# Performance work log

Hardware: AMD Instinct MI355X
Metric: run time of the kernel (lower is better)

Reference implementation:

```python
import jax, jax.numpy as jnp
import numpy as np

N = 30000
DEG = 16
E_RAND = N * DEG
E = E_RAND + N  # with self loops appended
T = 2
F_IN, H1, OUT = 128, 128, 64
NBSZ = 15
AGG = 0.8
NEG_SLOPE = 0.2


def setup_inputs() -> dict:
    key = jax.random.key(0)
    ks = jax.random.split(key, 10)
    x_all = jax.random.normal(ks[0], (T, N, F_IN), dtype=jnp.float32)
    # edges per snapshot: random edges + self loops (mirrors remove_self_loops + add_self_loops)
    loops = jnp.arange(N, dtype=jnp.int32)
    eis = []
    for t in range(T):
        src = jax.random.randint(jax.random.fold_in(ks[1], t), (E_RAND,), 0, N, dtype=jnp.int32)
        dst = jax.random.randint(jax.random.fold_in(ks[2], t), (E_RAND,), 0, N, dtype=jnp.int32)
        eis.append(jnp.stack([jnp.concatenate([src, loops]), jnp.concatenate([dst, loops])]))
    edge_index_all = jnp.stack(eis)  # [T, 2, E]
    def glorot(k, shape):
        fan = shape[0] + shape[-1]
        s = jnp.sqrt(6.0 / fan)
        return jax.random.uniform(k, shape, jnp.float32, -s, s)
    W1 = glorot(ks[3], (F_IN, 2 * H1))
    att1 = glorot(ks[4], (1, 1, 4 * H1))   # [1, heads=1, 2*out_neurons]
    b1 = jnp.zeros((2 * H1,), jnp.float32)
    W2 = glorot(ks[5], (H1, 2 * OUT))
    att2 = glorot(ks[6], (1, 1, 4 * OUT))
    b2 = jnp.zeros((2 * OUT,), jnp.float32)
    return {"x_all": x_all, "edge_index_all": edge_index_all,
            "W1": W1, "att1": att1, "b1": b1, "W2": W2, "att2": att2, "b2": b2}


def _conv(x, edge_index, W, att, b, C):
    """One DGIBConv (heads=1, Bernoulli distribution, diag reparam, eval mode).
    Returns (node_out [N,C], ixz scalar, structure_kl scalar)."""
    h = x @ W                                    # [N, 2C]
    src, dst = edge_index[0], edge_index[1]
    x_j = h[src]                                 # [E, 2C] per-edge gather (source)
    x_i = h[dst]                                 # [E, 2C] target
    a = att[0, 0]                                # [4C]
    logits = jnp.sum(x_i * a[:2 * C], -1) + jnp.sum(x_j * a[2 * C:], -1)  # [E]
    logits = jax.nn.leaky_relu(logits, NEG_SLOPE)
    # Bernoulli branch: softmax of ones over segments == 1/deg(dst)
    deg = jax.ops.segment_sum(jnp.ones_like(logits), dst, num_segments=N)  # [N]
    norm = 1.0 / deg[dst]
    p = jnp.clip(jax.nn.sigmoid(logits), 0.01, 0.99)  # posterior Bernoulli probs
    alpha = p * norm
    aggr = jax.ops.segment_sum(x_j * alpha[:, None], dst, num_segments=N) + b  # [N, 2C]
    # diag reparam: mean || std-logit split; Gaussian prior N(0, I)
    mu = aggr[:, :C]
    std = jax.nn.softplus(aggr[:, C:]) + 1e-10
    kl = -jnp.log(std) + 0.5 * (std * std + mu * mu) - 0.5  # KL(N(mu,std)||N(0,1)) per dim
    ixz = jnp.mean(jnp.sum(kl, -1))
    # structure KL: Bernoulli(p) || Bernoulli(logits = 1/nbsz)
    q = jax.nn.sigmoid(jnp.float32(1.0 / NBSZ))
    skl = jnp.mean(p * jnp.log(p / q) + (1.0 - p) * jnp.log((1.0 - p) / (1.0 - q)))
    return mu, ixz, skl


def _layer(x_list, edge_index_all, W, att, b, C):
    """Temporal DGIBConv.forward: per-snapshot conv + weighted temporal fusion."""
    outs, ixzs, skls = [], [], []
    for t in range(T):
        out, ixz, skl = _conv(x_list[t], edge_index_all[t], W, att, b, C)
        if t > 0:
            w = jax.nn.sigmoid(jnp.arange(t, dtype=jnp.float32))[:, None, None]  # [t,1,1]
            prev = jnp.stack(outs[:t])                                           # [t,N,C]
            out = jnp.sum(w * prev, 0) / t * AGG + out * (1.0 - AGG)
        outs.append(out)
        ixzs.append(ixz)
        skls.append(skl)
    return outs, jnp.mean(jnp.stack(ixzs)), jnp.mean(jnp.stack(skls))


def reference(x_all, edge_index_all, W1, att1, b1, W2, att2, b2):
    xs = [x_all[t] for t in range(T)]
    h1, ixz1, skl1 = _layer(xs, edge_index_all, W1, att1, b1, H1)
    h1 = [jax.nn.relu(h) for h in h1]  # with_relu=True, eval -> dropout is identity
    h2, ixz2, skl2 = _layer(h1, edge_index_all, W2, att2, b2, OUT)
    out = jnp.stack(h2)                # [T, N, OUT]
    ixz_mean = (ixz1 + ixz2) / 2.0
    skl_mean = (skl1 + skl2) / 2.0
    return out, ixz_mean, skl_mean
```

## Files before the change

### kernel.cpp

```cpp
#include <hip/hip_runtime.h>
#include <hip/hip_bf16.h>

#define N_NODES 30000
#define N_EDGES 510000
#define K_DIM   128
#define ABLK    7500
#define EBLK    997

typedef short bf16x8 __attribute__((ext_vector_type(8)));
typedef float f32x4  __attribute__((ext_vector_type(4)));
typedef float f32x2  __attribute__((ext_vector_type(2)));
typedef unsigned int u32x2 __attribute__((ext_vector_type(2)));

__device__ __forceinline__ unsigned short f2bf(float f) {
  __hip_bfloat16 h = __float2bfloat16(f);
  return *(unsigned short*)&h;
}

__global__ void transpose_w_kernel(const float* __restrict__ W1, unsigned short* __restrict__ Wt1,
                                   const float* __restrict__ W2, unsigned short* __restrict__ Wt2) {
  int i = blockIdx.x * blockDim.x + threadIdx.x;
  if (i < 128 * 256) {
    int k = i >> 8, m = i & 255;
    Wt1[m * 128 + k] = f2bf(W1[i]);
  } else if (i < 128 * 256 + 128 * 128) {
    int j = i - 128 * 256;
    int k = j >> 7, m = j & 127;
    Wt2[m * 128 + k] = f2bf(W2[j]);
  }
}

__global__ void deg_kernel(const int* __restrict__ ei, int* __restrict__ deg0,
                           int* __restrict__ deg1, int e) {
  int i = blockIdx.x * blockDim.x + threadIdx.x;
  if (i < 2 * e) {
    int t = i >= e ? 1 : 0;
    int j = i - t * e;
    int d = ei[(size_t)t * 2 * e + e + j];
    atomicAdd(&(t ? deg1 : deg0)[d], 1);
  }
}

__global__ __launch_bounds__(1024) void scan_kernel(const int* __restrict__ deg0, int* __restrict__ off0,
                                                    int* __restrict__ cur0, float* __restrict__ rn0,
                                                    const int* __restrict__ deg1, int* __restrict__ off1,
                                                    int* __restrict__ cur1, float* __restrict__ rn1,
                                                    int n) {
  const int* deg = blockIdx.x ? deg1 : deg0;
  int* off = blockIdx.x ? off1 : off0;
  int* cur = blockIdx.x ? cur1 : cur0;
  float* rn = blockIdx.x ? rn1 : rn0;
  const int CHUNK = 30;
  __shared__ int wsum[16];
  int tid = threadIdx.x;
  int base = tid * CHUNK;
  int sum = 0;
  for (int i = 0; i < CHUNK; i++)
    if (base + i < n) sum += deg[base + i];
  int lane = tid & 63, wid = tid >> 6;
  int incl = sum;
#pragma unroll
  for (int o = 1; o < 64; o <<= 1) {
    int v = __shfl_up(incl, o);
    if (lane >= o) incl += v;
  }
  if (lane == 63) wsum[wid] = incl;
  __syncthreads();
  if (tid == 0) {
    int run = 0;
    for (int w = 0; w < 16; w++) { int v = wsum[w]; wsum[w] = run; run += v; }
  }
  __syncthreads();
  int run = incl - sum + wsum[wid];
  for (int i = 0; i < CHUNK; i++) {
    if (base + i < n) {
      int dg = deg[base + i];
      off[base + i] = run;
      cur[base + i] = run;
      rn[base + i] = 1.0f / (float)dg;
      run += dg;
    }
  }
}

__global__ void scatter_kernel(const int* __restrict__ ei,
                               int* __restrict__ cur0, int* __restrict__ cur1,
                               unsigned int* __restrict__ csr0, unsigned int* __restrict__ csr1, int e) {
  int i = blockIdx.x * blockDim.x + threadIdx.x;
  if (i < 2 * e) {
    int t = i >= e ? 1 : 0;
    int j = i - t * e;
    int s = ei[(size_t)t * 2 * e + j];
    int d = ei[(size_t)t * 2 * e + e + j];
    int* cur = t ? cur1 : cur0;
    unsigned int* csr = t ? csr1 : csr0;
    int p = atomicAdd(&cur[d], 1);
    csr[p] = (unsigned int)s | ((unsigned int)d << 16);
  }
}

template<int M, bool F32IN>
__global__ __launch_bounds__(256) void gemm_kernel(const void* __restrict__ X0v,
                                                   const void* __restrict__ X1v,
                                                   const short* __restrict__ Wt,
                                                   unsigned char* __restrict__ H0,
                                                   unsigned char* __restrict__ H1,
                                                   const float* __restrict__ att,
                                                   float* __restrict__ si0, float* __restrict__ si1,
                                                   float* __restrict__ sj0, float* __restrict__ sj1,
                                                   int nrows) {
  int t = blockIdx.y;
  const void* Xv = t ? X1v : X0v;
  unsigned char* Hf8 = t ? H1 : H0;
  float* s_i = t ? si1 : si0;
  float* s_j = t ? sj1 : sj0;

  int wave = blockIdx.x * 4 + (threadIdx.x >> 6);
  int lane = threadIdx.x & 63;
  if (wave * 16 >= nrows) return;
  int m16 = lane & 15, quad = lane >> 4;

  bf16x8 a[4];
  size_t arow = (size_t)(wave * 16 + m16) * K_DIM + quad * 8;
  if constexpr (F32IN) {
    const float* X = (const float*)Xv;
#pragma unroll
    for (int kc = 0; kc < 4; kc++) {
      f32x4 lo = *(const f32x4*)(X + arow + kc * 32);
      f32x4 hi = *(const f32x4*)(X + arow + kc * 32 + 4);
#pragma unroll
      for (int j = 0; j < 4; j++) {
        ((unsigned short*)&a[kc])[j]     = f2bf(lo[j]);
        ((unsigned short*)&a[kc])[4 + j] = f2bf(hi[j]);
      }
    }
  } else {
    const short* X = (const short*)Xv;
#pragma unroll
    for (int kc = 0; kc < 4; kc++) a[kc] = *(const bf16x8*)(X + arow + kc * 32);
  }

  float sip[4] = {0.f, 0.f, 0.f, 0.f}, sjp[4] = {0.f, 0.f, 0.f, 0.f};
#pragma unroll
  for (int nt = 0; nt < M / 16; nt++) {
    f32x4 acc = {0.f, 0.f, 0.f, 0.f};
    size_t brow = (size_t)(nt * 16 + m16) * K_DIM + quad * 8;
#pragma unroll
    for (int kc = 0; kc < 4; kc++) {
      bf16x8 b = *(const bf16x8*)(Wt + brow + kc * 32);
      acc = __builtin_amdgcn_mfma_f32_16x16x32_bf16(a[kc], b, acc, 0, 0, 0);
    }
    int col = nt * 16 + m16;
    float aA = att[col], aB = att[M + col];
#pragma unroll
    for (int r = 0; r < 4; r++) {
      int row = wave * 16 + quad * 4 + r;
      int pk = __builtin_amdgcn_cvt_pk_fp8_f32(acc[r], acc[r], 0, false);
      Hf8[(size_t)row * M + col] = (unsigned char)pk;
      sip[r] += acc[r] * aA;
      sjp[r] += acc[r] * aB;
    }
  }
#pragma unroll
  for (int o = 1; o < 16; o <<= 1) {
#pragma unroll
    for (int r = 0; r < 4; r++) {
      sip[r] += __shfl_xor(sip[r], o);
      sjp[r] += __shfl_xor(sjp[r], o);
    }
  }
  if (m16 == 0) {
#pragma unroll
    for (int r = 0; r < 4; r++) {
      int row = wave * 16 + quad * 4 + r;
      s_i[row] = sip[r];
      s_j[row] = sjp[r];
    }
  }
}

__global__ __launch_bounds__(256) void edge_kernel(const unsigned int* __restrict__ csr_0,
                                                   const unsigned int* __restrict__ csr_1,
                                                   const float* __restrict__ rn0, const float* __restrict__ rn1,
                                                   const float* __restrict__ si0, const float* __restrict__ si1,
                                                   const float* __restrict__ sj0, const float* __restrict__ sj1,
                                                   u32x2* __restrict__ iw0, u32x2* __restrict__ iw1,
                                                   float* __restrict__ epart,
                                                   int e) {
  int t = blockIdx.y;
  const unsigned int* csr = t ? csr_1 : csr_0;
  const float* rn = t ? rn1 : rn0;
  const float* s_i = t ? si1 : si0;
  const float* s_j = t ? sj1 : sj0;
  u32x2* iw = t ? iw1 : iw0;

  const float q   = 1.0f / (1.0f + __expf(-(1.0f / 15.0f)));
  const float lq  = __logf(q);
  const float l1q = __logf(1.0f - q);

  __shared__ float red[4];
  float skl = 0.f;
  int p0 = (blockIdx.x * 256 + threadIdx.x) * 2;
#pragma unroll
  for (int u = 0; u < 2; u++) {
    int p = p0 + u;
    if (p < e) {
      unsigned int sd = csr[p];
      int s = (int)(sd & 0xffffu);
      int dd = (int)(sd >> 16);
      float lg = s_i[dd] + s_j[s];
      lg = lg > 0.f ? lg : 0.2f * lg;
      float pv = 1.0f / (1.0f + __expf(-lg));
      pv = fminf(fmaxf(pv, 0.01f), 0.99f);
      skl += pv * (__logf(pv) - lq) + (1.0f - pv) * (__logf(1.0f - pv) - l1q);
      float w = pv * rn[dd];
      u32x2 o;
      o[0] = (unsigned int)s;
      o[1] = __float_as_uint(w);
      iw[p] = o;
    }
  }
  int lane = threadIdx.x & 63, wid = threadIdx.x >> 6;
#pragma unroll
  for (int o = 32; o > 0; o >>= 1) skl += __shfl_xor(skl, o);
  if (lane == 0) red[wid] = skl;
  __syncthreads();
  if (threadIdx.x == 0) epart[t * EBLK + blockIdx.x] = red[0] + red[1] + red[2] + red[3];
}

template<int M>
__global__ __launch_bounds__(256, 6) void aggr_kernel(const unsigned char* __restrict__ H0,
                                                   const unsigned char* __restrict__ H1,
                                                   const u32x2* __restrict__ iw0, const u32x2* __restrict__ iw1,
                                                   const int* __restrict__ off0, const int* __restrict__ off1,
                                                   const int* __restrict__ deg0, const int* __restrict__ deg1,
                                                   const float* __restrict__ bias,
                                                   float* __restrict__ mu0, float* __restrict__ mu1,
                                                   float* __restrict__ apart,
                                                   int n) {
  constexpr int C = M / 2;
  constexpr int LPR = M / 8;
  constexpr int L2LPR = (M == 256) ? 5 : 4;
  constexpr int EPL = 64 / LPR;
  constexpr int NL = 8;
  constexpr int U = NL * EPL;

  int t = blockIdx.y;
  const unsigned char* Hf8 = t ? H1 : H0;
  const u32x2* iw = t ? iw1 : iw0;
  const int* off = t ? off1 : off0;
  const int* deg = t ? deg1 : deg0;
  float* mu = t ? mu1 : mu0;

  __shared__ float red_i[4];
  int wid = threadIdx.x >> 6, lane = threadIdx.x & 63;
  int wave = blockIdx.x * 4 + wid;
  float ixz = 0.f;

  if (wave < n) {
    int d     = __builtin_amdgcn_readfirstlane(deg[wave]);
    int start = __builtin_amdgcn_readfirstlane(off[wave]);
    const u32x2* iwp = iw + start;
    int sub = lane & (LPR - 1);
    int g   = lane >> L2LPR;
    int c0  = sub * 8;
    const unsigned char* hbase = Hf8 + c0;

    f32x2 acc[4];
#pragma unroll
    for (int k = 0; k < 4; k++) acc[k] = {0.f, 0.f};

    for (int e0 = 0; e0 < d; e0 += U) {
      u32x2 iwl[NL];
#pragma unroll
      for (int l = 0; l < NL; l++) {
        int e = e0 + l * EPL + g;
        iwl[l] = iwp[e < d ? e : d - 1];
      }
      u32x2 hv[NL];
#pragma unroll
      for (int l = 0; l < NL; l++)
        hv[l] = *(const u32x2*)(hbase + (size_t)iwl[l][0] * M);
#pragma unroll
      for (int l = 0; l < NL; l++) {
        int e = e0 + l * EPL + g;
        float wf = (e < d) ? __uint_as_float(iwl[l][1]) : 0.f;
        f32x2 wv = {wf, wf};
        f32x2 d0 = __builtin_amdgcn_cvt_pk_f32_fp8((int)hv[l][0], false);
        f32x2 d1 = __builtin_amdgcn_cvt_pk_f32_fp8((int)hv[l][0], true);
        f32x2 d2 = __builtin_amdgcn_cvt_pk_f32_fp8((int)hv[l][1], false);
        f32x2 d3 = __builtin_amdgcn_cvt_pk_f32_fp8((int)hv[l][1], true);
        acc[0] = d0 * wv + acc[0];
        acc[1] = d1 * wv + acc[1];
        acc[2] = d2 * wv + acc[2];
        acc[3] = d3 * wv + acc[3];
      }
    }

#pragma unroll
    for (int o = LPR; o < 64; o <<= 1) {
#pragma unroll
      for (int j = 0; j < 4; j++) {
        acc[j][0] += __shfl_xor(acc[j][0], o);
        acc[j][1] += __shfl_xor(acc[j][1], o);
      }
    }

    if (lane < LPR) {
      if (c0 < C) {
        f32x4 mv[2];
#pragma unroll
        for (int j = 0; j < 4; j++) {
          float a0 = acc[j][0] + bias[c0 + 2 * j];
          float a1 = acc[j][1] + bias[c0 + 2 * j + 1];
          ixz += 0.5f * (a0 * a0 + a1 * a1) - 1.0f;
          mv[j >> 1][(j & 1) * 2]     = a0;
          mv[j >> 1][(j & 1) * 2 + 1] = a1;
        }
        *(f32x4*)(mu + (size_t)wave * C + c0)     = mv[0];
        *(f32x4*)(mu + (size_t)wave * C + c0 + 4) = mv[1];
      } else {
#pragma unroll
        for (int j = 0; j < 4; j++) {
#pragma unroll
          for (int h = 0; h < 2; h++) {
            float a = acc[j][h] + bias[c0 + 2 * j + h];
            float sp = (a > 20.f) ? a : log1pf(__expf(a));
            sp += 1e-10f;
            ixz += -__logf(sp) + 0.5f * sp * sp;
          }
        }
      }
    }
  }
#pragma unroll
  for (int o = 32; o > 0; o >>= 1) ixz += __shfl_xor(ixz, o);
  if (lane == 0) red_i[wid] = ixz;
  __syncthreads();
  if (threadIdx.x == 0)
    apart[t * ABLK + blockIdx.x] = red_i[0] + red_i[1] + red_i[2] + red_i[3];
}

__global__ void fuse1_kernel(const float* __restrict__ mu0, const float* __restrict__ mu1,
                             __hip_bfloat16* __restrict__ x0, __hip_bfloat16* __restrict__ x1, int n) {
  int i = blockIdx.x * blockDim.x + threadIdx.x;
  if (i < n) {
    float m0 = mu0[i], m1 = mu1[i];
    x0[i] = __float2bfloat16(fmaxf(m0, 0.f));
    x1[i] = __float2bfloat16(fmaxf(0.4f * m0 + 0.2f * m1, 0.f));
  }
}

__global__ void fuse2_kernel(const float* __restrict__ mu0, const float* __restrict__ mu1,
                             float* __restrict__ out, int n) {
  int i = blockIdx.x * blockDim.x + threadIdx.x;
  if (i < n) {
    float m0 = mu0[i], m1 = mu1[i];
    out[i] = m0;
    out[n + i] = 0.4f * m0 + 0.2f * m1;
  }
}

__global__ __launch_bounds__(1024) void reduce_kernel(const float* __restrict__ a1,
                                                      const float* __restrict__ a2,
                                                      const float* __restrict__ e1,
                                                      const float* __restrict__ e2,
                                                      float* __restrict__ out2) {
  __shared__ float ri[16], rs[16];
  float ixz = 0.f, skl = 0.f;
  for (int i = threadIdx.x; i < 2 * ABLK; i += 1024) ixz += a1[i] + a2[i];
  for (int i = threadIdx.x; i < 2 * EBLK; i += 1024) skl += e1[i] + e2[i];
  int lane = threadIdx.x & 63, wid = threadIdx.x >> 6;
#pragma unroll
  for (int o = 32; o > 0; o >>= 1) {
    ixz += __shfl_xor(ixz, o);
    skl += __shfl_xor(skl, o);
  }
  if (lane == 0) { ri[wid] = ixz; rs[wid] = skl; }
  __syncthreads();
  if (threadIdx.x == 0) {
    float si = 0.f, ss = 0.f;
    for (int w = 0; w < 16; w++) { si += ri[w]; ss += rs[w]; }
    out2[0] = si / (4.0f * (float)N_NODES);
    out2[1] = ss / (4.0f * (float)N_EDGES);
  }
}

extern "C" void kernel_launch(void* const* d_in, const int* in_sizes, int n_in,
                              void* d_out, int out_size, void* d_ws, size_t ws_size,
                              hipStream_t stream) {
  const float* x_all = (const float*)d_in[0];
  const int* ei      = (const int*)d_in[1];
  const float* W1    = (const float*)d_in[2];
  const float* att1  = (const float*)d_in[3];
  const float* b1    = (const float*)d_in[4];
  const float* W2    = (const float*)d_in[5];
  const float* att2  = (const float*)d_in[6];
  const float* b2    = (const float*)d_in[7];
  float* out         = (float*)d_out;

  char* ws = (char*)d_ws;
  size_t off = 0;
  auto alloc = [&](size_t bytes) {
    char* p = ws + off;
    off = (off + bytes + 255) & ~(size_t)255;
    return p;
  };
  unsigned short* wt1  = (unsigned short*)alloc(256 * 128 * sizeof(short));
  unsigned short* wt2  = (unsigned short*)alloc(128 * 128 * sizeof(short));
  unsigned char* hf8_0 = (unsigned char*)alloc((size_t)N_NODES * 256);
  unsigned char* hf8_1 = (unsigned char*)alloc((size_t)N_NODES * 256);
  float* si0   = (float*)alloc(N_NODES * sizeof(float));
  float* si1   = (float*)alloc(N_NODES * sizeof(float));
  float* sj0   = (float*)alloc(N_NODES * sizeof(float));
  float* sj1   = (float*)alloc(N_NODES * sizeof(float));
  float* mu1_0 = (float*)alloc((size_t)N_NODES * 128 * sizeof(float));
  float* mu1_1 = (float*)alloc((size_t)N_NODES * 128 * sizeof(float));
  char* x2region = alloc((size_t)N_NODES * 256 * sizeof(short));
  __hip_bfloat16* x2_0 = (__hip_bfloat16*)x2region;
  __hip_bfloat16* x2_1 = x2_0 + (size_t)N_NODES * 128;
  u32x2* iwp[2] = {(u32x2*)x2region, (u32x2*)x2region + N_EDGES};
  float* mu2_0 = mu1_0;
  float* mu2_1 = mu1_0 + (size_t)N_NODES * 64;
  int* degp[2]  = {(int*)alloc(N_NODES * 4), (int*)alloc(N_NODES * 4)};
  int* offp[2]  = {(int*)alloc(N_NODES * 4), (int*)alloc(N_NODES * 4)};
  int* curp[2]  = {(int*)alloc(N_NODES * 4), (int*)alloc(N_NODES * 4)};
  float* rnp[2] = {(float*)alloc(N_NODES * 4), (float*)alloc(N_NODES * 4)};
  unsigned int* csrp[2] = {(unsigned int*)alloc((size_t)N_EDGES * 4),
                           (unsigned int*)alloc((size_t)N_EDGES * 4)};
  float* apart1 = (float*)alloc(2 * ABLK * sizeof(float));
  float* apart2 = (float*)alloc(2 * ABLK * sizeof(float));
  float* epart1 = (float*)alloc(2 * EBLK * sizeof(float));
  float* epart2 = (float*)alloc(2 * EBLK * sizeof(float));

  hipMemsetAsync(degp[0], 0, N_NODES * 4, stream);
  hipMemsetAsync(degp[1], 0, N_NODES * 4, stream);

  transpose_w_kernel<<<192, 256, 0, stream>>>(W1, wt1, W2, wt2);

  deg_kernel<<<(2 * N_EDGES + 255) / 256, 256, 0, stream>>>(ei, degp[0], degp[1], N_EDGES);
  scan_kernel<<<2, 1024, 0, stream>>>(degp[0], offp[0], curp[0], rnp[0],
                                      degp[1], offp[1], curp[1], rnp[1], N_NODES);
  scatter_kernel<<<(2 * N_EDGES + 255) / 256, 256, 0, stream>>>(ei, curp[0], curp[1],
                                                                csrp[0], csrp[1], N_EDGES);

  dim3 ggrid(469, 2), egrid(EBLK, 2), agrid(ABLK, 2);

  const float* x0 = x_all;
  const float* x1 = x_all + (size_t)N_NODES * K_DIM;
  gemm_kernel<256, true><<<ggrid, 256, 0, stream>>>(x0, x1, (const short*)wt1, hf8_0, hf8_1,
                                                    att1, si0, si1, sj0, sj1, N_NODES);
  edge_kernel<<<egrid, 256, 0, stream>>>(csrp[0], csrp[1], rnp[0], rnp[1],
                                         si0, si1, sj0, sj1, iwp[0], iwp[1], epart1, N_EDGES);
  aggr_kernel<256><<<agrid, 256, 0, stream>>>(hf8_0, hf8_1, iwp[0], iwp[1], offp[0], offp[1],
                                              degp[0], degp[1], b1, mu1_0, mu1_1, apart1, N_NODES);
  fuse1_kernel<<<(N_NODES * 128 + 255) / 256, 256, 0, stream>>>(mu1_0, mu1_1, x2_0, x2_1, N_NODES * 128);

  gemm_kernel<128, false><<<ggrid, 256, 0, stream>>>(x2_0, x2_1, (const short*)wt2, hf8_0, hf8_1,
                                                     att2, si0, si1, sj0, sj1, N_NODES);
  edge_kernel<<<egrid, 256, 0, stream>>>(csrp[0], csrp[1], rnp[0], rnp[1],
                                         si0, si1, sj0, sj1, iwp[0], iwp[1], epart2, N_EDGES);
  aggr_kernel<128><<<agrid, 256, 0, stream>>>(hf8_0, hf8_1, iwp[0], iwp[1], offp[0], offp[1],
                                              degp[0], degp[1], b2, mu2_0, mu2_1, apart2, N_NODES);
  fuse2_kernel<<<(N_NODES * 64 + 255) / 256, 256, 0, stream>>>(mu2_0, mu2_1, out, N_NODES * 64);
  reduce_kernel<<<1, 1024, 0, stream>>>(apart1, apart2, epart1, epart2, out + (size_t)2 * N_NODES * 64);
}
```

Before: 607.6 us.

## Replace pull-based CSR gather aggregation with source-sorted push scatter using bf16 atomics

New measurement: 1.501 ms. +147.0%, slower.

```diff
diff --git a/kernel.cpp b/kernel.cpp
--- a/kernel.cpp
+++ b/kernel.cpp
@@ -1,20 +1,43 @@
 #include <hip/hip_runtime.h>
 #include <hip/hip_bf16.h>
+
+#ifndef __has_builtin
+#define __has_builtin(x) 0
+#endif
 
 #define N_NODES 30000
 #define N_EDGES 510000
 #define K_DIM   128
 #define ABLK    7500
 #define EBLK    997
+#define FB1     15000
+#define FB2     7500
 
 typedef short bf16x8 __attribute__((ext_vector_type(8)));
 typedef float f32x4  __attribute__((ext_vector_type(4)));
 typedef float f32x2  __attribute__((ext_vector_type(2)));
 typedef unsigned int u32x2 __attribute__((ext_vector_type(2)));
+typedef short s16x2 __attribute__((ext_vector_type(2)));
 
 __device__ __forceinline__ unsigned short f2bf(float f) {
   __hip_bfloat16 h = __float2bfloat16(f);
   return *(unsigned short*)&h;
+}
+__device__ __forceinline__ float bf2f(unsigned short u) {
+  __hip_bfloat16 h = *(__hip_bfloat16*)&u;
+  return __bfloat162float(h);
+}
+
+__device__ __forceinline__ void atom_pk_bf16(unsigned int* addr, float lo, float hi) {
+  __hip_bfloat162 b2(__float2bfloat16(lo), __float2bfloat16(hi));
+#if __has_builtin(__builtin_amdgcn_global_atomic_fadd_v2bf16)
+  union { __hip_bfloat162 b; s16x2 v; } u;
+  u.b = b2;
+  __builtin_amdgcn_global_atomic_fadd_v2bf16(
+      (__attribute__((address_space(1))) s16x2*)addr, u.v);
+#else
+  unsafeAtomicAdd((__hip_bfloat162*)addr, b2);
+#endif
 }
 
 __global__ void transpose_w_kernel(const float* __restrict__ W1, unsigned short* __restrict__ Wt1,
@@ -30,25 +53,29 @@
   }
 }
 
-__global__ void deg_kernel(const int* __restrict__ ei, int* __restrict__ deg0,
-                           int* __restrict__ deg1, int e) {
+__global__ void deg_kernel(const int* __restrict__ ei,
+                           int* __restrict__ deg0, int* __restrict__ deg1,
+                           int* __restrict__ degS0, int* __restrict__ degS1, int e) {
   int i = blockIdx.x * blockDim.x + threadIdx.x;
   if (i < 2 * e) {
     int t = i >= e ? 1 : 0;
     int j = i - t * e;
+    int s = ei[(size_t)t * 2 * e + j];
     int d = ei[(size_t)t * 2 * e + e + j];
     atomicAdd(&(t ? deg1 : deg0)[d], 1);
-  }
-}
-
-__global__ __launch_bounds__(1024) void scan_kernel(const int* __restrict__ deg0, int* __restrict__ off0,
-                                                    int* __restrict__ cur0, float* __restrict__ rn0,
-                                                    const int* __restrict__ deg1, int* __restrict__ off1,
-                                                    int* __restrict__ cur1, float* __restrict__ rn1,
+    atomicAdd(&(t ? degS1 : degS0)[s], 1);
+  }
+}
+
+__global__ __launch_bounds__(1024) void scan_kernel(const int* __restrict__ degS0, int* __restrict__ offS0, int* __restrict__ curS0,
+                                                    const int* __restrict__ degS1, int* __restrict__ offS1, int* __restrict__ curS1,
+                                                    const int* __restrict__ deg0, float* __restrict__ rn0,
+                                                    const int* __restrict__ deg1, float* __restrict__ rn1,
                                                     int n) {
+  const int* degS = blockIdx.x ? degS1 : degS0;
+  int* off = blockIdx.x ? offS1 : offS0;
+  int* cur = blockIdx.x ? curS1 : curS0;
   const int* deg = blockIdx.x ? deg1 : deg0;
-  int* off = blockIdx.x ? off1 : off0;
-  int* cur = blockIdx.x ? cur1 : cur0;
   float* rn = blockIdx.x ? rn1 : rn0;
   const int CHUNK = 30;
   __shared__ int wsum[16];
@@ -56,7 +83,7 @@
   int base = tid * CHUNK;
   int sum = 0;
   for (int i = 0; i < CHUNK; i++)
-    if (base + i < n) sum += deg[base + i];
+    if (base + i < n) sum += degS[base + i];
   int lane = tid & 63, wid = tid >> 6;
   int incl = sum;
 #pragma unroll
@@ -74,27 +101,27 @@
   int run = incl - sum + wsum[wid];
   for (int i = 0; i < CHUNK; i++) {
     if (base + i < n) {
-      int dg = deg[base + i];
+      int dg = degS[base + i];
       off[base + i] = run;
       cur[base + i] = run;
-      rn[base + i] = 1.0f / (float)dg;
+      rn[base + i] = 1.0f / (float)deg[base + i];
       run += dg;
     }
   }
 }
 
 __global__ void scatter_kernel(const int* __restrict__ ei,
-                               int* __restrict__ cur0, int* __restrict__ cur1,
-                               unsigned int* __restrict__ csr0, unsigned int* __restrict__ csr1, int e) {
+                               int* __restrict__ curS0, int* __restrict__ curS1,
+                               unsigned int* __restrict__ csrS0, unsigned int* __restrict__ csrS1, int e) {
   int i = blockIdx.x * blockDim.x + threadIdx.x;
   if (i < 2 * e) {
     int t = i >= e ? 1 : 0;
     int j = i - t * e;
     int s = ei[(size_t)t * 2 * e + j];
     int d = ei[(size_t)t * 2 * e + e + j];
-    int* cur = t ? cur1 : cur0;
-    unsigned int* csr = t ? csr1 : csr0;
-    int p = atomicAdd(&cur[d], 1);
+    int* cur = t ? curS1 : curS0;
+    unsigned int* csr = t ? csrS1 : csrS0;
+    int p = atomicAdd(&cur[s], 1);
     csr[p] = (unsigned int)s | ((unsigned int)d << 16);
   }
 }
@@ -215,7 +242,7 @@
       skl += pv * (__logf(pv) - lq) + (1.0f - pv) * (__logf(1.0f - pv) - l1q);
       float w = pv * rn[dd];
       u32x2 o;
-      o[0] = (unsigned int)s;
+      o[0] = (unsigned int)dd;
       o[1] = __float_as_uint(w);
       iw[p] = o;
     }
@@ -229,136 +256,112 @@
 }
 
 template<int M>
-__global__ __launch_bounds__(256, 6) void aggr_kernel(const unsigned char* __restrict__ H0,
+__global__ __launch_bounds__(256) void scat_kernel(const unsigned char* __restrict__ H0,
                                                    const unsigned char* __restrict__ H1,
                                                    const u32x2* __restrict__ iw0, const u32x2* __restrict__ iw1,
-                                                   const int* __restrict__ off0, const int* __restrict__ off1,
-                                                   const int* __restrict__ deg0, const int* __restrict__ deg1,
-                                                   const float* __restrict__ bias,
-                                                   float* __restrict__ mu0, float* __restrict__ mu1,
-                                                   float* __restrict__ apart,
+                                                   const int* __restrict__ offS0, const int* __restrict__ offS1,
+                                                   const int* __restrict__ degS0, const int* __restrict__ degS1,
+                                                   unsigned short* __restrict__ A0, unsigned short* __restrict__ A1v,
                                                    int n) {
-  constexpr int C = M / 2;
-  constexpr int LPR = M / 8;
-  constexpr int L2LPR = (M == 256) ? 5 : 4;
-  constexpr int EPL = 64 / LPR;
-  constexpr int NL = 8;
-  constexpr int U = NL * EPL;
-
   int t = blockIdx.y;
   const unsigned char* Hf8 = t ? H1 : H0;
   const u32x2* iw = t ? iw1 : iw0;
-  const int* off = t ? off1 : off0;
-  const int* deg = t ? deg1 : deg0;
-  float* mu = t ? mu1 : mu0;
-
-  __shared__ float red_i[4];
+  const int* offS = t ? offS1 : offS0;
+  const int* degS = t ? degS1 : degS0;
+  unsigned int* A = (unsigned int*)(t ? A1v : A0);
+
   int wid = threadIdx.x >> 6, lane = threadIdx.x & 63;
-  int wave = blockIdx.x * 4 + wid;
-  float ixz = 0.f;
-
-  if (wave < n) {
-    int d     = __builtin_amdgcn_readfirstlane(deg[wave]);
-    int start = __builtin_amdgcn_readfirstlane(off[wave]);
-    const u32x2* iwp = iw + start;
-    int sub = lane & (LPR - 1);
-    int g   = lane >> L2LPR;
-    int c0  = sub * 8;
-    const unsigned char* hbase = Hf8 + c0;
-
-    f32x2 acc[4];
-#pragma unroll
-    for (int k = 0; k < 4; k++) acc[k] = {0.f, 0.f};
-
-    for (int e0 = 0; e0 < d; e0 += U) {
-      u32x2 iwl[NL];
-#pragma unroll
-      for (int l = 0; l < NL; l++) {
-        int e = e0 + l * EPL + g;
-        iwl[l] = iwp[e < d ? e : d - 1];
+  int s = blockIdx.x * 4 + wid;
+  if (s >= n) return;
+  int d     = __builtin_amdgcn_readfirstlane(degS[s]);
+  int start = __builtin_amdgcn_readfirstlane(offS[s]);
+
+  float h0, h1, h2 = 0.f, h3 = 0.f;
+  if constexpr (M == 256) {
+    unsigned int hv = *(const unsigned int*)(Hf8 + (size_t)s * M + lane * 4);
+    f32x2 lo = __builtin_amdgcn_cvt_pk_f32_fp8((int)hv, false);
+    f32x2 hi = __builtin_amdgcn_cvt_pk_f32_fp8((int)hv, true);
+    h0 = lo[0]; h1 = lo[1]; h2 = hi[0]; h3 = hi[1];
+  } else {
+    unsigned int hv = *(const unsigned short*)(Hf8 + (size_t)s * M + lane * 2);
+    f32x2 lo = __builtin_amdgcn_cvt_pk_f32_fp8((int)hv, false);
+    h0 = lo[0]; h1 = lo[1];
+  }
+
+  const u32x2* iwp = iw + start;
+  for (int e0 = 0; e0 < d; e0 += 64) {
+    int ee = e0 + lane;
+    u32x2 iwv = iwp[ee < d ? ee : d - 1];
+    int cnt = min(d - e0, 64);
+    for (int e = 0; e < cnt; e++) {
+      int dst = __builtin_amdgcn_readlane((int)iwv[0], e);
+      float w = __uint_as_float(__builtin_amdgcn_readlane((int)iwv[1], e));
+      if constexpr (M == 256) {
+        unsigned int* row = A + (size_t)dst * (M / 2);
+        atom_pk_bf16(row + lane * 2,     h0 * w, h1 * w);
+        atom_pk_bf16(row + lane * 2 + 1, h2 * w, h3 * w);
+      } else {
+        atom_pk_bf16(A + (size_t)dst * (M / 2) + lane, h0 * w, h1 * w);
       }
-      u32x2 hv[NL];
-#pragma unroll
-      for (int l = 0; l < NL; l++)
-        hv[l] = *(const u32x2*)(hbase + (size_t)iwl[l][0] * M);
-#pragma unroll
-      for (int l = 0; l < NL; l++) {
-        int e = e0 + l * EPL + g;
-        float wf = (e < d) ? __uint_as_float(iwl[l][1]) : 0.f;
-        f32x2 wv = {wf, wf};
-        f32x2 d0 = __builtin_amdgcn_cvt_pk_f32_fp8((int)hv[l][0], false);
-        f32x2 d1 = __builtin_amdgcn_cvt_pk_f32_fp8((int)hv[l][0], true);
-        f32x2 d2 = __builtin_amdgcn_cvt_pk_f32_fp8((int)hv[l][1], false);
-        f32x2 d3 = __builtin_amdgcn_cvt_pk_f32_fp8((int)hv[l][1], true);
-        acc[0] = d0 * wv + acc[0];
-        acc[1] = d1 * wv + acc[1];
-        acc[2] = d2 * wv + acc[2];
-        acc[3] = d3 * wv + acc[3];
-      }
-    }
-
-#pragma unroll
-    for (int o = LPR; o < 64; o <<= 1) {
-#pragma unroll
-      for (int j = 0; j < 4; j++) {
-        acc[j][0] += __shfl_xor(acc[j][0], o);
-        acc[j][1] += __shfl_xor(acc[j][1], o);
-      }
-    }
-
-    if (lane < LPR) {
-      if (c0 < C) {
-        f32x4 mv[2];
-#pragma unroll
-        for (int j = 0; j < 4; j++) {
-          float a0 = acc[j][0] + bias[c0 + 2 * j];
-          float a1 = acc[j][1] + bias[c0 + 2 * j + 1];
-          ixz += 0.5f * (a0 * a0 + a1 * a1) - 1.0f;
-          mv[j >> 1][(j & 1) * 2]     = a0;
-          mv[j >> 1][(j & 1) * 2 + 1] = a1;
-        }
-        *(f32x4*)(mu + (size_t)wave * C + c0)     = mv[0];
-        *(f32x4*)(mu + (size_t)wave * C + c0 + 4) = mv[1];
-      } else {
-#pragma unroll
-        for (int j = 0; j < 4; j++) {
-#pragma unroll
-          for (int h = 0; h < 2; h++) {
-            float a = acc[j][h] + bias[c0 + 2 * j + h];
-            float sp = (a > 20.f) ? a : log1pf(__expf(a));
-            sp += 1e-10f;
-            ixz += -__logf(sp) + 0.5f * sp * sp;
-          }
-        }
-      }
-    }
-  }
+    }
+  }
+}
+
+__global__ __launch_bounds__(256) void fuse1_kernel(const unsigned short* __restrict__ A0,
+                                                    const unsigned short* __restrict__ A1v,
+                                                    const float* __restrict__ b,
+                                                    __hip_bfloat16* __restrict__ x0,
+                                                    __hip_bfloat16* __restrict__ x1,
+                                                    float* __restrict__ apart) {
+  __shared__ float red[4];
+  int i = blockIdx.x * 256 + threadIdx.x;
+  int v = i >> 7, c = i & 127;
+  float bm = b[c], bs = b[128 + c];
+  const unsigned short* r0 = A0 + (size_t)v * 256;
+  const unsigned short* r1 = A1v + (size_t)v * 256;
+  float a0m = bf2f(r0[c]) + bm, a0s = bf2f(r0[128 + c]) + bs;
+  float a1m = bf2f(r1[c]) + bm, a1s = bf2f(r1[128 + c]) + bs;
+  float sp0 = (a0s > 20.f) ? a0s : log1pf(__expf(a0s)); sp0 += 1e-10f;
+  float sp1 = (a1s > 20.f) ? a1s : log1pf(__expf(a1s)); sp1 += 1e-10f;
+  float ixz = 0.5f * (a0m * a0m + a1m * a1m) - 1.0f
+            - __logf(sp0) + 0.5f * sp0 * sp0
+            - __logf(sp1) + 0.5f * sp1 * sp1;
+  x0[(size_t)v * 128 + c] = __float2bfloat16(fmaxf(a0m, 0.f));
+  x1[(size_t)v * 128 + c] = __float2bfloat16(fmaxf(0.4f * a0m + 0.2f * a1m, 0.f));
+  int lane = threadIdx.x & 63, wid = threadIdx.x >> 6;
 #pragma unroll
   for (int o = 32; o > 0; o >>= 1) ixz += __shfl_xor(ixz, o);
-  if (lane == 0) red_i[wid] = ixz;
-  __syncthreads();
-  if (threadIdx.x == 0)
-    apart[t * ABLK + blockIdx.x] = red_i[0] + red_i[1] + red_i[2] + red_i[3];
-}
-
-__global__ void fuse1_kernel(const float* __restrict__ mu0, const float* __restrict__ mu1,
-                             __hip_bfloat16* __restrict__ x0, __hip_bfloat16* __restrict__ x1, int n) {
-  int i = blockIdx.x * blockDim.x + threadIdx.x;
-  if (i < n) {
-    float m0 = mu0[i], m1 = mu1[i];
-    x0[i] = __float2bfloat16(fmaxf(m0, 0.f));
-    x1[i] = __float2bfloat16(fmaxf(0.4f * m0 + 0.2f * m1, 0.f));
-  }
-}
-
-__global__ void fuse2_kernel(const float* __restrict__ mu0, const float* __restrict__ mu1,
-                             float* __restrict__ out, int n) {
-  int i = blockIdx.x * blockDim.x + threadIdx.x;
-  if (i < n) {
-    float m0 = mu0[i], m1 = mu1[i];
-    out[i] = m0;
-    out[n + i] = 0.4f * m0 + 0.2f * m1;
-  }
+  if (lane == 0) red[wid] = ixz;
+  __syncthreads();
+  if (threadIdx.x == 0) apart[blockIdx.x] = red[0] + red[1] + red[2] + red[3];
+}
+
+__global__ __launch_bounds__(256) void fuse2_kernel(const unsigned short* __restrict__ A0,
+                                                    const unsigned short* __restrict__ A1v,
+                                                    const float* __restrict__ b,
+                                                    float* __restrict__ out,
+                                                    float* __restrict__ apart) {
+  __shared__ float red[4];
+  int i = blockIdx.x * 256 + threadIdx.x;
+  int v = i >> 6, c = i & 63;
+  float bm = b[c], bs = b[64 + c];
+  const unsigned short* r0 = A0 + (size_t)v * 128;
+  const unsigned short* r1 = A1v + (size_t)v * 128;
+  float a0m = bf2f(r0[c]) + bm, a0s = bf2f(r0[64 + c]) + bs;
+  float a1m = bf2f(r1[c]) + bm, a1s = bf2f(r1[64 + c]) + bs;
+  float sp0 = (a0s > 20.f) ? a0s : log1pf(__expf(a0s)); sp0 += 1e-10f;
+  float sp1 = (a1s > 20.f) ? a1s : log1pf(__expf(a1s)); sp1 += 1e-10f;
+  float ixz = 0.5f * (a0m * a0m + a1m * a1m) - 1.0f
+            - __logf(sp0) + 0.5f * sp0 * sp0
+            - __logf(sp1) + 0.5f * sp1 * sp1;
+  out[i] = a0m;
+  out[(size_t)N_NODES * 64 + i] = 0.4f * a0m + 0.2f * a1m;
+  int lane = threadIdx.x & 63, wid = threadIdx.x >> 6;
+#pragma unroll
+  for (int o = 32; o > 0; o >>= 1) ixz += __shfl_xor(ixz, o);
+  if (lane == 0) red[wid] = ixz;
+  __syncthreads();
+  if (threadIdx.x == 0) apart[blockIdx.x] = red[0] + red[1] + red[2] + red[3];
 }
 
 __global__ __launch_bounds__(1024) void reduce_kernel(const float* __restrict__ a1,
@@ -368,7 +371,8 @@
                                                       float* __restrict__ out2) {
   __shared__ float ri[16], rs[16];
   float ixz = 0.f, skl = 0.f;
-  for (int i = threadIdx.x; i < 2 * ABLK; i += 1024) ixz += a1[i] + a2[i];
+  for (int i = threadIdx.x; i < FB1; i += 1024) ixz += a1[i];
+  for (int i = threadIdx.x; i < FB2; i += 1024) ixz += a2[i];
   for (int i = threadIdx.x; i < 2 * EBLK; i += 1024) skl += e1[i] + e2[i];
   int lane = threadIdx.x & 63, wid = threadIdx.x >> 6;
 #pragma unroll
@@ -414,35 +418,42 @@
   float* si1   = (float*)alloc(N_NODES * sizeof(float));
   float* sj0   = (float*)alloc(N_NODES * sizeof(float));
   float* sj1   = (float*)alloc(N_NODES * sizeof(float));
-  float* mu1_0 = (float*)alloc((size_t)N_NODES * 128 * sizeof(float));
-  float* mu1_1 = (float*)alloc((size_t)N_NODES * 128 * sizeof(float));
+  char* Aregion = alloc((size_t)2 * N_NODES * 256 * sizeof(short));
+  unsigned short* A1_0 = (unsigned short*)Aregion;
+  unsigned short* A1_1 = A1_0 + (size_t)N_NODES * 256;
+  unsigned short* A2_0 = A1_0;
+  unsigned short* A2_1 = A1_0 + (size_t)N_NODES * 128;
   char* x2region = alloc((size_t)N_NODES * 256 * sizeof(short));
   __hip_bfloat16* x2_0 = (__hip_bfloat16*)x2region;
   __hip_bfloat16* x2_1 = x2_0 + (size_t)N_NODES * 128;
   u32x2* iwp[2] = {(u32x2*)x2region, (u32x2*)x2region + N_EDGES};
-  float* mu2_0 = mu1_0;
-  float* mu2_1 = mu1_0 + (size_t)N_NODES * 64;
   int* degp[2]  = {(int*)alloc(N_NODES * 4), (int*)alloc(N_NODES * 4)};
-  int* offp[2]  = {(int*)alloc(N_NODES * 4), (int*)alloc(N_NODES * 4)};
-  int* curp[2]  = {(int*)alloc(N_NODES * 4), (int*)alloc(N_NODES * 4)};
+  int* degSp[2] = {(int*)alloc(N_NODES * 4), (int*)alloc(N_NODES * 4)};
+  int* offSp[2] = {(int*)alloc(N_NODES * 4), (int*)alloc(N_NODES * 4)};
+  int* curSp[2] = {(int*)alloc(N_NODES * 4), (int*)alloc(N_NODES * 4)};
   float* rnp[2] = {(float*)alloc(N_NODES * 4), (float*)alloc(N_NODES * 4)};
-  unsigned int* csrp[2] = {(unsigned int*)alloc((size_t)N_EDGES * 4),
-                           (unsigned int*)alloc((size_t)N_EDGES * 4)};
-  float* apart1 = (float*)alloc(2 * ABLK * sizeof(float));
-  float* apart2 = (float*)alloc(2 * ABLK * sizeof(float));
+  unsigned int* csrSp[2] = {(unsigned int*)alloc((size_t)N_EDGES * 4),
+                            (unsigned int*)alloc((size_t)N_EDGES * 4)};
+  float* apart1 = (float*)alloc(FB1 * sizeof(float));
+  float* apart2 = (float*)alloc(FB2 * sizeof(float));
   float* epart1 = (float*)alloc(2 * EBLK * sizeof(float));
   float* epart2 = (float*)alloc(2 * EBLK * sizeof(float));
 
   hipMemsetAsync(degp[0], 0, N_NODES * 4, stream);
   hipMemsetAsync(degp[1], 0, N_NODES * 4, stream);
+  hipMemsetAsync(degSp[0], 0, N_NODES * 4, stream);
+  hipMemsetAsync(degSp[1], 0, N_NODES * 4, stream);
+  hipMemsetAsync(Aregion, 0, (size_t)2 * N_NODES * 256 * sizeof(short), stream);
 
   transpose_w_kernel<<<192, 256, 0, stream>>>(W1, wt1, W2, wt2);
 
-  deg_kernel<<<(2 * N_EDGES + 255) / 256, 256, 0, stream>>>(ei, degp[0], degp[1], N_EDGES);
-  scan_kernel<<<2, 1024, 0, stream>>>(degp[0], offp[0], curp[0], rnp[0],
-                                      degp[1], offp[1], curp[1], rnp[1], N_NODES);
-  scatter_kernel<<<(2 * N_EDGES + 255) / 256, 256, 0, stream>>>(ei, curp[0], curp[1],
-                                                                csrp[0], csrp[1], N_EDGES);
+  deg_kernel<<<(2 * N_EDGES + 255) / 256, 256, 0, stream>>>(ei, degp[0], degp[1],
+                                                            degSp[0], degSp[1], N_EDGES);
+  scan_kernel<<<2, 1024, 0, stream>>>(degSp[0], offSp[0], curSp[0],
+                                      degSp[1], offSp[1], curSp[1],
+                                      degp[0], rnp[0], degp[1], rnp[1], N_NODES);
+  scatter_kernel<<<(2 * N_EDGES + 255) / 256, 256, 0, stream>>>(ei, curSp[0], curSp[1],
+                                                                csrSp[0], csrSp[1], N_EDGES);
 
   dim3 ggrid(469, 2), egrid(EBLK, 2), agrid(ABLK, 2);
 
@@ -450,18 +461,19 @@
   const float* x1 = x_all + (size_t)N_NODES * K_DIM;
   gemm_kernel<256, true><<<ggrid, 256, 0, stream>>>(x0, x1, (const short*)wt1, hf8_0, hf8_1,
                                                     att1, si0, si1, sj0, sj1, N_NODES);
-  edge_kernel<<<egrid, 256, 0, stream>>>(csrp[0], csrp[1], rnp[0], rnp[1],
+  edge_kernel<<<egrid, 256, 0, stream>>>(csrSp[0], csrSp[1], rnp[0], rnp[1],
                                          si0, si1, sj0, sj1, iwp[0], iwp[1], epart1, N_EDGES);
-  aggr_kernel<256><<<agrid, 256, 0, stream>>>(hf8_0, hf8_1, iwp[0], iwp[1], offp[0], offp[1],
-                                              degp[0], degp[1], b1, mu1_0, mu1_1, apart1, N_NODES);
-  fuse1_kernel<<<(N_NODES * 128 + 255) / 256, 256, 0, stream>>>(mu1_0, mu1_1, x2_0, x2_1, N_NODES * 128);
+  scat_kernel<256><<<agrid, 256, 0, stream>>>(hf8_0, hf8_1, iwp[0], iwp[1], offSp[0], offSp[1],
+                                              degSp[0], degSp[1], A1_0, A1_1, N_NODES);
+  fuse1_kernel<<<FB1, 256, 0, stream>>>(A1_0, A1_1, b1, x2_0, x2_1, apart1);
+  hipMemsetAsync(Aregion, 0, (size_t)2 * N_NODES * 128 * sizeof(short), stream);
 
   gemm_kernel<128, false><<<ggrid, 256, 0, stream>>>(x2_0, x2_1, (const short*)wt2, hf8_0, hf8_1,
                                                      att2, si0, si1, sj0, sj1, N_NODES);
-  edge_kernel<<<egrid, 256, 0, stream>>>(csrp[0], csrp[1], rnp[0], rnp[1],
+  edge_kernel<<<egrid, 256, 0, stream>>>(csrSp[0], csrSp[1], rnp[0], rnp[1],
                                          si0, si1, sj0, sj1, iwp[0], iwp[1], epart2, N_EDGES);
-  aggr_kernel<128><<<agrid, 256, 0, stream>>>(hf8_0, hf8_1, iwp[0], iwp[1], offp[0], offp[1],
-                                              degp[0], degp[1], b2, mu2_0, mu2_1, apart2, N_NODES);
-  fuse2_kernel<<<(N_NODES * 64 + 255) / 256, 256, 0, stream>>>(mu2_0, mu2_1, out, N_NODES * 64);
+  scat_kernel<128><<<agrid, 256, 0, stream>>>(hf8_0, hf8_1, iwp[0], iwp[1], offSp[0], offSp[1],
+                                              degSp[0], degSp[1], A2_0, A2_1, N_NODES);
+  fuse2_kernel<<<FB2, 256, 0, stream>>>(A2_0, A2_1, b2, out, apart2);
   reduce_kernel<<<1, 1024, 0, stream>>>(apart1, apart2, epart1, epart2, out + (size_t)2 * N_NODES * 64);
 }
```

## Fuse layer-1 temporal mix into GEMM, pack edge weights to bf16, split aggregation channels

Applied to the files above, without the earlier changes.

After: 636.5 us. 4.8% more time.

```diff
diff --git a/kernel.cpp b/kernel.cpp
--- a/kernel.cpp
+++ b/kernel.cpp
@@ -99,7 +99,7 @@
   }
 }
 
-template<int M, bool F32IN>
+template<int M, int MODE>
 __global__ __launch_bounds__(256) void gemm_kernel(const void* __restrict__ X0v,
                                                    const void* __restrict__ X1v,
                                                    const short* __restrict__ Wt,
@@ -110,7 +110,6 @@
                                                    float* __restrict__ sj0, float* __restrict__ sj1,
                                                    int nrows) {
   int t = blockIdx.y;
-  const void* Xv = t ? X1v : X0v;
   unsigned char* Hf8 = t ? H1 : H0;
   float* s_i = t ? si1 : si0;
   float* s_j = t ? sj1 : sj0;
@@ -122,8 +121,8 @@
 
   bf16x8 a[4];
   size_t arow = (size_t)(wave * 16 + m16) * K_DIM + quad * 8;
-  if constexpr (F32IN) {
-    const float* X = (const float*)Xv;
+  if constexpr (MODE == 0) {
+    const float* X = (const float*)(t ? X1v : X0v);
 #pragma unroll
     for (int kc = 0; kc < 4; kc++) {
       f32x4 lo = *(const f32x4*)(X + arow + kc * 32);
@@ -135,9 +134,24 @@
       }
     }
   } else {
-    const short* X = (const short*)Xv;
-#pragma unroll
-    for (int kc = 0; kc < 4; kc++) a[kc] = *(const bf16x8*)(X + arow + kc * 32);
+    const float* Xa = (const float*)X0v;
+    const float* Xb = (const float*)X1v;
+#pragma unroll
+    for (int kc = 0; kc < 4; kc++) {
+      f32x4 lo = *(const f32x4*)(Xa + arow + kc * 32);
+      f32x4 hi = *(const f32x4*)(Xa + arow + kc * 32 + 4);
+      if (t) {
+        f32x4 lo1 = *(const f32x4*)(Xb + arow + kc * 32);
+        f32x4 hi1 = *(const f32x4*)(Xb + arow + kc * 32 + 4);
+        lo = lo * 0.4f + lo1 * 0.2f;
+        hi = hi * 0.4f + hi1 * 0.2f;
+      }
+#pragma unroll
+      for (int j = 0; j < 4; j++) {
+        ((unsigned short*)&a[kc])[j]     = f2bf(fmaxf(lo[j], 0.f));
+        ((unsigned short*)&a[kc])[4 + j] = f2bf(fmaxf(hi[j], 0.f));
+      }
+    }
   }
 
   float sip[4] = {0.f, 0.f, 0.f, 0.f}, sjp[4] = {0.f, 0.f, 0.f, 0.f};
@@ -184,7 +198,7 @@
                                                    const float* __restrict__ rn0, const float* __restrict__ rn1,
                                                    const float* __restrict__ si0, const float* __restrict__ si1,
                                                    const float* __restrict__ sj0, const float* __restrict__ sj1,
-                                                   u32x2* __restrict__ iw0, u32x2* __restrict__ iw1,
+                                                   unsigned int* __restrict__ iw0, unsigned int* __restrict__ iw1,
                                                    float* __restrict__ epart,
                                                    int e) {
   int t = blockIdx.y;
@@ -192,7 +206,7 @@
   const float* rn = t ? rn1 : rn0;
   const float* s_i = t ? si1 : si0;
   const float* s_j = t ? sj1 : sj0;
-  u32x2* iw = t ? iw1 : iw0;
+  unsigned int* iw = t ? iw1 : iw0;
 
   const float q   = 1.0f / (1.0f + __expf(-(1.0f / 15.0f)));
   const float lq  = __logf(q);
@@ -214,10 +228,7 @@
       pv = fminf(fmaxf(pv, 0.01f), 0.99f);
       skl += pv * (__logf(pv) - lq) + (1.0f - pv) * (__logf(1.0f - pv) - l1q);
       float w = pv * rn[dd];
-      u32x2 o;
-      o[0] = (unsigned int)s;
-      o[1] = __float_as_uint(w);
-      iw[p] = o;
+      iw[p] = (unsigned int)s | ((unsigned int)f2bf(w) << 16);
     }
   }
   int lane = threadIdx.x & 63, wid = threadIdx.x >> 6;
@@ -229,9 +240,10 @@
 }
 
 template<int M>
-__global__ __launch_bounds__(256, 6) void aggr_kernel(const unsigned char* __restrict__ H0,
+__global__ __launch_bounds__(256) void aggr_kernel(const unsigned char* __restrict__ H0,
                                                    const unsigned char* __restrict__ H1,
-                                                   const u32x2* __restrict__ iw0, const u32x2* __restrict__ iw1,
+                                                   const unsigned int* __restrict__ iw0,
+                                                   const unsigned int* __restrict__ iw1,
                                                    const int* __restrict__ off0, const int* __restrict__ off1,
                                                    const int* __restrict__ deg0, const int* __restrict__ deg1,
                                                    const float* __restrict__ bias,
@@ -239,15 +251,17 @@
                                                    float* __restrict__ apart,
                                                    int n) {
   constexpr int C = M / 2;
-  constexpr int LPR = M / 8;
-  constexpr int L2LPR = (M == 256) ? 5 : 4;
+  constexpr int HB = M / 2;
+  constexpr int LPR = HB / 8;
+  constexpr int L2LPR = (M == 256) ? 4 : 3;
   constexpr int EPL = 64 / LPR;
-  constexpr int NL = 8;
+  constexpr int NL = 4;
   constexpr int U = NL * EPL;
 
-  int t = blockIdx.y;
+  int y = blockIdx.y;
+  int t = y >> 1, q = y & 1;
   const unsigned char* Hf8 = t ? H1 : H0;
-  const u32x2* iw = t ? iw1 : iw0;
+  const unsigned int* iw = t ? iw1 : iw0;
   const int* off = t ? off1 : off0;
   const int* deg = t ? deg1 : deg0;
   float* mu = t ? mu1 : mu0;
@@ -260,18 +274,17 @@
   if (wave < n) {
     int d     = __builtin_amdgcn_readfirstlane(deg[wave]);
     int start = __builtin_amdgcn_readfirstlane(off[wave]);
-    const u32x2* iwp = iw + start;
+    const unsigned int* iwp = iw + start;
     int sub = lane & (LPR - 1);
     int g   = lane >> L2LPR;
-    int c0  = sub * 8;
-    const unsigned char* hbase = Hf8 + c0;
+    const unsigned char* hbase = Hf8 + q * HB + sub * 8;
 
     f32x2 acc[4];
 #pragma unroll
     for (int k = 0; k < 4; k++) acc[k] = {0.f, 0.f};
 
     for (int e0 = 0; e0 < d; e0 += U) {
-      u32x2 iwl[NL];
+      unsigned int iwl[NL];
 #pragma unroll
       for (int l = 0; l < NL; l++) {
         int e = e0 + l * EPL + g;
@@ -280,11 +293,11 @@
       u32x2 hv[NL];
 #pragma unroll
       for (int l = 0; l < NL; l++)
-        hv[l] = *(const u32x2*)(hbase + (size_t)iwl[l][0] * M);
+        hv[l] = *(const u32x2*)(hbase + (size_t)(iwl[l] & 0xffffu) * M);
 #pragma unroll
       for (int l = 0; l < NL; l++) {
         int e = e0 + l * EPL + g;
-        float wf = (e < d) ? __uint_as_float(iwl[l][1]) : 0.f;
+        float wf = (e < d) ? __uint_as_float(iwl[l] & 0xffff0000u) : 0.f;
         f32x2 wv = {wf, wf};
         f32x2 d0 = __builtin_amdgcn_cvt_pk_f32_fp8((int)hv[l][0], false);
         f32x2 d1 = __builtin_amdgcn_cvt_pk_f32_fp8((int)hv[l][0], true);
@@ -307,24 +320,25 @@
     }
 
     if (lane < LPR) {
-      if (c0 < C) {
+      int ch0 = q * HB + sub * 8;
+      if (q == 0) {
         f32x4 mv[2];
 #pragma unroll
         for (int j = 0; j < 4; j++) {
-          float a0 = acc[j][0] + bias[c0 + 2 * j];
-          float a1 = acc[j][1] + bias[c0 + 2 * j + 1];
+          float a0 = acc[j][0] + bias[ch0 + 2 * j];
+          float a1 = acc[j][1] + bias[ch0 + 2 * j + 1];
           ixz += 0.5f * (a0 * a0 + a1 * a1) - 1.0f;
           mv[j >> 1][(j & 1) * 2]     = a0;
           mv[j >> 1][(j & 1) * 2 + 1] = a1;
         }
-        *(f32x4*)(mu + (size_t)wave * C + c0)     = mv[0];
-        *(f32x4*)(mu + (size_t)wave * C + c0 + 4) = mv[1];
+        *(f32x4*)(mu + (size_t)wave * C + ch0)     = mv[0];
+        *(f32x4*)(mu + (size_t)wave * C + ch0 + 4) = mv[1];
       } else {
 #pragma unroll
         for (int j = 0; j < 4; j++) {
 #pragma unroll
           for (int h = 0; h < 2; h++) {
-            float a = acc[j][h] + bias[c0 + 2 * j + h];
+            float a = acc[j][h] + bias[ch0 + 2 * j + h];
             float sp = (a > 20.f) ? a : log1pf(__expf(a));
             sp += 1e-10f;
             ixz += -__logf(sp) + 0.5f * sp * sp;
@@ -338,17 +352,7 @@
   if (lane == 0) red_i[wid] = ixz;
   __syncthreads();
   if (threadIdx.x == 0)
-    apart[t * ABLK + blockIdx.x] = red_i[0] + red_i[1] + red_i[2] + red_i[3];
-}
-
-__global__ void fuse1_kernel(const float* __restrict__ mu0, const float* __restrict__ mu1,
-                             __hip_bfloat16* __restrict__ x0, __hip_bfloat16* __restrict__ x1, int n) {
-  int i = blockIdx.x * blockDim.x + threadIdx.x;
-  if (i < n) {
-    float m0 = mu0[i], m1 = mu1[i];
-    x0[i] = __float2bfloat16(fmaxf(m0, 0.f));
-    x1[i] = __float2bfloat16(fmaxf(0.4f * m0 + 0.2f * m1, 0.f));
-  }
+    apart[y * ABLK + blockIdx.x] = red_i[0] + red_i[1] + red_i[2] + red_i[3];
 }
 
 __global__ void fuse2_kernel(const float* __restrict__ mu0, const float* __restrict__ mu1,
@@ -368,7 +372,7 @@
                                                       float* __restrict__ out2) {
   __shared__ float ri[16], rs[16];
   float ixz = 0.f, skl = 0.f;
-  for (int i = threadIdx.x; i < 2 * ABLK; i += 1024) ixz += a1[i] + a2[i];
+  for (int i = threadIdx.x; i < 4 * ABLK; i += 1024) ixz += a1[i] + a2[i];
   for (int i = threadIdx.x; i < 2 * EBLK; i += 1024) skl += e1[i] + e2[i];
   int lane = threadIdx.x & 63, wid = threadIdx.x >> 6;
 #pragma unroll
@@ -416,20 +420,18 @@
   float* sj1   = (float*)alloc(N_NODES * sizeof(float));
   float* mu1_0 = (float*)alloc((size_t)N_NODES * 128 * sizeof(float));
   float* mu1_1 = (float*)alloc((size_t)N_NODES * 128 * sizeof(float));
-  char* x2region = alloc((size_t)N_NODES * 256 * sizeof(short));
-  __hip_bfloat16* x2_0 = (__hip_bfloat16*)x2region;
-  __hip_bfloat16* x2_1 = x2_0 + (size_t)N_NODES * 128;
-  u32x2* iwp[2] = {(u32x2*)x2region, (u32x2*)x2region + N_EDGES};
   float* mu2_0 = mu1_0;
   float* mu2_1 = mu1_0 + (size_t)N_NODES * 64;
+  unsigned int* iwp[2] = {(unsigned int*)alloc((size_t)N_EDGES * 4),
+                          (unsigned int*)alloc((size_t)N_EDGES * 4)};
   int* degp[2]  = {(int*)alloc(N_NODES * 4), (int*)alloc(N_NODES * 4)};
   int* offp[2]  = {(int*)alloc(N_NODES * 4), (int*)alloc(N_NODES * 4)};
   int* curp[2]  = {(int*)alloc(N_NODES * 4), (int*)alloc(N_NODES * 4)};
   float* rnp[2] = {(float*)alloc(N_NODES * 4), (float*)alloc(N_NODES * 4)};
   unsigned int* csrp[2] = {(unsigned int*)alloc((size_t)N_EDGES * 4),
                            (unsigned int*)alloc((size_t)N_EDGES * 4)};
-  float* apart1 = (float*)alloc(2 * ABLK * sizeof(float));
-  float* apart2 = (float*)alloc(2 * ABLK * sizeof(float));
+  float* apart1 = (float*)alloc(4 * ABLK * sizeof(float));
+  float* apart2 = (float*)alloc(4 * ABLK * sizeof(float));
   float* epart1 = (float*)alloc(2 * EBLK * sizeof(float));
   float* epart2 = (float*)alloc(2 * EBLK * sizeof(float));
 
@@ -444,20 +446,19 @@
   scatter_kernel<<<(2 * N_EDGES + 255) / 256, 256, 0, stream>>>(ei, curp[0], curp[1],
                                                                 csrp[0], csrp[1], N_EDGES);
 
-  dim3 ggrid(469, 2), egrid(EBLK, 2), agrid(ABLK, 2);
+  dim3 ggrid(469, 2), egrid(EBLK, 2), agrid(ABLK, 4);
 
   const float* x0 = x_all;
   const float* x1 = x_all + (size_t)N_NODES * K_DIM;
-  gemm_kernel<256, true><<<ggrid, 256, 0, stream>>>(x0, x1, (const short*)wt1, hf8_0, hf8_1,
-                                                    att1, si0, si1, sj0, sj1, N_NODES);
+  gemm_kernel<256, 0><<<ggrid, 256, 0, stream>>>(x0, x1, (const short*)wt1, hf8_0, hf8_1,
+                                                 att1, si0, si1, sj0, sj1, N_NODES);
   edge_kernel<<<egrid, 256, 0, stream>>>(csrp[0], csrp[1], rnp[0], rnp[1],
                                          si0, si1, sj0, sj1, iwp[0], iwp[1], epart1, N_EDGES);
   aggr_kernel<256><<<agrid, 256, 0, stream>>>(hf8_0, hf8_1, iwp[0], iwp[1], offp[0], offp[1],
                                               degp[0], degp[1], b1, mu1_0, mu1_1, apart1, N_NODES);
-  fuse1_kernel<<<(N_NODES * 128 + 255) / 256, 256, 0, stream>>>(mu1_0, mu1_1, x2_0, x2_1, N_NODES * 128);
-
-  gemm_kernel<128, false><<<ggrid, 256, 0, stream>>>(x2_0, x2_1, (const short*)wt2, hf8_0, hf8_1,
-                                                     att2, si0, si1, sj0, sj1, N_NODES);
+
+  gemm_kernel<128, 1><<<ggrid, 256, 0, stream>>>(mu1_0, mu1_1, (const short*)wt2, hf8_0, hf8_1,
+                                                 att2, si0, si1, sj0, sj1, N_NODES);
   edge_kernel<<<egrid, 256, 0, stream>>>(csrp[0], csrp[1], rnp[0], rnp[1],
                                          si0, si1, sj0, sj1, iwp[0], iwp[1], epart2, N_EDGES);
   aggr_kernel<128><<<agrid, 256, 0, stream>>>(hf8_0, hf8_1, iwp[0], iwp[1], offp[0], offp[1],
```
